# Performance work log

Measured on AMD Instinct MI355X. Metric: run time of the kernel, lower is better.

## Reference

```python
import jax, jax.numpy as jnp
import numpy as np

N = 1024
D_X = 128
D_Y = 128
NUM_STEPS = 200


def setup_inputs() -> dict:
    key = jax.random.key(0)
    k1, k2, k3, k4, k5 = jax.random.split(key, 5)
    init_samples_x = jax.random.normal(k1, (N, D_X), dtype=jnp.float32)
    init_samples_y = jax.random.normal(k2, (N, D_Y), dtype=jnp.float32)
    mean_final = jax.random.normal(k3, (D_X,), dtype=jnp.float32)
    # variance must be positive and bounded away from zero
    var_final = jax.random.uniform(k4, (D_X,), dtype=jnp.float32, minval=0.25, maxval=0.75)
    gammas = jnp.linspace(1e-3, 1e-2, NUM_STEPS, dtype=jnp.float32)
    # pre-generated per-step Gaussian noise (replaces torch.randn inside the loop)
    noise = jax.random.normal(k5, (NUM_STEPS, N, D_X), dtype=jnp.float32)
    return {
        "init_samples_x": init_samples_x,
        "init_samples_y": init_samples_y,
        "mean_final": mean_final,
        "var_final": var_final,
        "gammas": gammas,
        "noise": noise,
    }


def reference(init_samples_x, init_samples_y, mean_final, var_final, gammas, noise):
    """Faithful JAX port of Langevin.record_init_langevin.

    grad_gauss(x, m, v) = -(x - m) / v
    per step k:
        t_old = x + gamma_k * grad_gauss(x)
        x     = t_old + sqrt(2*gamma_k) * z_k
        t_new = x + gamma_k * grad_gauss(x)
        record x, y, t_old - t_new
    """
    num_steps = gammas.shape[0]
    n = init_samples_x.shape[0]

    def step(x, inp):
        gamma, z = inp
        t_old = x + gamma * (-(x - mean_final) / var_final)
        x_new = t_old + jnp.sqrt(2.0 * gamma) * z
        t_new = x_new + gamma * (-(x_new - mean_final) / var_final)
        return x_new, (x_new, t_old - t_new)

    _, (xs, outs) = jax.lax.scan(step, init_samples_x, (gammas, noise))
    # scan stacks along leading (step) axis -> [S, N, D]; match torch layout [N, S, D]
    x_tot = jnp.transpose(xs, (1, 0, 2))
    out = jnp.transpose(outs, (1, 0, 2))
    # y is constant across steps; the torch loop just replicates it
    y_tot = jnp.broadcast_to(init_samples_y[:, None, :], (n, num_steps, init_samples_y.shape[1]))
    steps_expanded = jnp.broadcast_to(
        jnp.arange(num_steps, dtype=jnp.int32)[None, :, None], (n, num_steps, 1)
    )
    return x_tot, y_tot, out, steps_expanded
```

## Files before the change

kernel.cpp:

```cpp
#include <hip/hip_runtime.h>
#include <math.h>

constexpr int N  = 1024;
constexpr int D  = 128;
constexpr int S  = 200;
constexpr int D2 = D / 2;

__global__ __launch_bounds__(256, 4) void langevin_kernel(
    const float2* __restrict__ x0,
    const float2* __restrict__ y0,
    const float2* __restrict__ mean,
    const float2* __restrict__ var,
    const float*  __restrict__ gammas,
    const float2* __restrict__ noise,
    float2* __restrict__ x_tot,
    float2* __restrict__ y_tot,
    float2* __restrict__ outp,
    float*  __restrict__ steps)
{
    __shared__ float sg[S];
    __shared__ float ss[S];
    for (int i = threadIdx.x; i < S; i += 256) {
        float g = gammas[i];
        sg[i] = g;
        ss[i] = sqrtf(2.0f * g);
    }
    __syncthreads();

    const int idx = blockIdx.x * 256 + threadIdx.x;
    const int n   = idx >> 6;
    const int dp  = idx & 63;

    float2 x       = x0[idx];
    const float2 y = y0[idx];
    const float2 m = mean[dp];
    const float2 v = var[dp];
    const float ivx = 1.0f / v.x;
    const float ivy = 1.0f / v.y;

    const float2* zp = noise + idx;
    float2* xq = x_tot + (size_t)n * (S * D2) + dp;
    float2* yq = y_tot + (size_t)n * (S * D2) + dp;
    float2* oq = outp  + (size_t)n * (S * D2) + dp;
    float*  sq = steps + (size_t)n * S;

    #pragma unroll 4
    for (int k = 0; k < S; ++k) {
        const float g = sg[k];
        const float s = ss[k];
        const float2 z = zp[(size_t)k * (N * D2)];

        const float gx = g * ivx;
        const float gy = g * ivy;

        const float tox = fmaf(-gx, x.x - m.x, x.x);
        const float toy = fmaf(-gy, x.y - m.y, x.y);
        x.x = fmaf(s, z.x, tox);
        x.y = fmaf(s, z.y, toy);
        const float tnx = fmaf(-gx, x.x - m.x, x.x);
        const float tny = fmaf(-gy, x.y - m.y, x.y);

        float2 o;
        o.x = tox - tnx;
        o.y = toy - tny;

        xq[(size_t)k * D2] = x;
        yq[(size_t)k * D2] = y;
        oq[(size_t)k * D2] = o;
        if (dp == 0) sq[k] = (float)k;
    }
}

extern "C" void kernel_launch(void* const* d_in, const int* in_sizes, int n_in,
                              void* d_out, int out_size, void* d_ws, size_t ws_size,
                              hipStream_t stream)
{
    const float* x0     = (const float*)d_in[0];
    const float* y0     = (const float*)d_in[1];
    const float* mean   = (const float*)d_in[2];
    const float* var    = (const float*)d_in[3];
    const float* gammas = (const float*)d_in[4];
    const float* noise  = (const float*)d_in[5];

    float* x_tot = (float*)d_out;
    float* y_tot = x_tot + (size_t)N * S * D;
    float* outp  = y_tot + (size_t)N * S * D;
    float* steps = outp  + (size_t)N * S * D;

    dim3 grid((N * D2) / 256);
    dim3 block(256);
    langevin_kernel<<<grid, block, 0, stream>>>(
        (const float2*)x0, (const float2*)y0, (const float2*)mean,
        (const float2*)var, gammas, (const float2*)noise,
        (float2*)x_tot, (float2*)y_tot, (float2*)outp, steps);
}
```

Before: 476.6 us.

## Split y/steps broadcast into separate blocks and software-prefetch noise with nontemporal ops

Adds N extra blocks that write the replicated y tensor with 16-byte nontemporal stores plus the step indices, removing that work from the Langevin chain threads. The chain threads now double-buffer noise loads eight steps ahead and use nontemporal loads and stores for the noise, x and out streams. The aim is better memory-level parallelism and less cache pollution on a purely bandwidth-bound kernel. Register use grows because of the prefetch buffers.

```diff
diff --git a/kernel.cpp b/kernel.cpp
--- a/kernel.cpp
+++ b/kernel.cpp
@@ -1,23 +1,45 @@
 #include <hip/hip_runtime.h>
 #include <math.h>
 
-constexpr int N  = 1024;
-constexpr int D  = 128;
-constexpr int S  = 200;
-constexpr int D2 = D / 2;
+constexpr int N   = 1024;
+constexpr int D   = 128;
+constexpr int S   = 200;
+constexpr int D2  = D / 2;
+constexpr int ND2 = N * D2;
+constexpr int CHAIN_BLOCKS = (N * D2) / 256;
+constexpr int PF  = 8;
+
+typedef float f2 __attribute__((ext_vector_type(2)));
+typedef float f4 __attribute__((ext_vector_type(4)));
 
 __global__ __launch_bounds__(256, 4) void langevin_kernel(
-    const float2* __restrict__ x0,
-    const float2* __restrict__ y0,
-    const float2* __restrict__ mean,
-    const float2* __restrict__ var,
-    const float*  __restrict__ gammas,
-    const float2* __restrict__ noise,
-    float2* __restrict__ x_tot,
-    float2* __restrict__ y_tot,
-    float2* __restrict__ outp,
-    float*  __restrict__ steps)
+    const f2* __restrict__ x0,
+    const f4* __restrict__ y0,
+    const f2* __restrict__ mean,
+    const f2* __restrict__ var,
+    const float* __restrict__ gammas,
+    const f2* __restrict__ noise,
+    f2* __restrict__ x_tot,
+    f4* __restrict__ y_tot,
+    f2* __restrict__ outp,
+    float* __restrict__ steps)
 {
+    if (blockIdx.x >= CHAIN_BLOCKS) {
+        const int n   = blockIdx.x - CHAIN_BLOCKS;
+        const int t   = threadIdx.x;
+        const int col = t & 31;
+        const int r0  = t >> 5;
+        const f4  yv  = y0[(size_t)n * 32 + col];
+        f4* yq = y_tot + (size_t)n * (S * 32);
+        #pragma unroll
+        for (int j = 0; j < S / 8; ++j) {
+            const int k = r0 + j * 8;
+            __builtin_nontemporal_store(yv, &yq[(size_t)k * 32 + col]);
+        }
+        if (t < S) steps[(size_t)n * S + t] = (float)t;
+        return;
+    }
+
     __shared__ float sg[S];
     __shared__ float ss[S];
     for (int i = threadIdx.x; i < S; i += 256) {
@@ -31,43 +53,53 @@
     const int n   = idx >> 6;
     const int dp  = idx & 63;
 
-    float2 x       = x0[idx];
-    const float2 y = y0[idx];
-    const float2 m = mean[dp];
-    const float2 v = var[dp];
+    f2 x        = x0[idx];
+    const f2 m  = mean[dp];
+    const f2 v  = var[dp];
     const float ivx = 1.0f / v.x;
     const float ivy = 1.0f / v.y;
 
-    const float2* zp = noise + idx;
-    float2* xq = x_tot + (size_t)n * (S * D2) + dp;
-    float2* yq = y_tot + (size_t)n * (S * D2) + dp;
-    float2* oq = outp  + (size_t)n * (S * D2) + dp;
-    float*  sq = steps + (size_t)n * S;
+    const f2* zp = noise + idx;
+    f2* xq = x_tot + (size_t)n * (S * D2) + dp;
+    f2* oq = outp  + (size_t)n * (S * D2) + dp;
 
-    #pragma unroll 4
-    for (int k = 0; k < S; ++k) {
-        const float g = sg[k];
-        const float s = ss[k];
-        const float2 z = zp[(size_t)k * (N * D2)];
+    f2 zb[PF];
+    #pragma unroll
+    for (int i = 0; i < PF; ++i)
+        zb[i] = __builtin_nontemporal_load(&zp[(size_t)i * ND2]);
 
-        const float gx = g * ivx;
-        const float gy = g * ivy;
+    #pragma unroll 1
+    for (int kb = 0; kb < S; kb += PF) {
+        f2 zn[PF];
+        if (kb + PF < S) {
+            #pragma unroll
+            for (int i = 0; i < PF; ++i)
+                zn[i] = __builtin_nontemporal_load(&zp[(size_t)(kb + PF + i) * ND2]);
+        }
+        #pragma unroll
+        for (int i = 0; i < PF; ++i) {
+            const int k = kb + i;
+            const float g = sg[k];
+            const float s = ss[k];
+            const float gx = g * ivx;
+            const float gy = g * ivy;
 
-        const float tox = fmaf(-gx, x.x - m.x, x.x);
-        const float toy = fmaf(-gy, x.y - m.y, x.y);
-        x.x = fmaf(s, z.x, tox);
-        x.y = fmaf(s, z.y, toy);
-        const float tnx = fmaf(-gx, x.x - m.x, x.x);
-        const float tny = fmaf(-gy, x.y - m.y, x.y);
+            const float tox = fmaf(-gx, x.x - m.x, x.x);
+            const float toy = fmaf(-gy, x.y - m.y, x.y);
+            x.x = fmaf(s, zb[i].x, tox);
+            x.y = fmaf(s, zb[i].y, toy);
+            const float tnx = fmaf(-gx, x.x - m.x, x.x);
+            const float tny = fmaf(-gy, x.y - m.y, x.y);
 
-        float2 o;
-        o.x = tox - tnx;
-        o.y = toy - tny;
+            f2 o;
+            o.x = tox - tnx;
+            o.y = toy - tny;
 
-        xq[(size_t)k * D2] = x;
-        yq[(size_t)k * D2] = y;
-        oq[(size_t)k * D2] = o;
-        if (dp == 0) sq[k] = (float)k;
+            __builtin_nontemporal_store(x, &xq[(size_t)k * D2]);
+            __builtin_nontemporal_store(o, &oq[(size_t)k * D2]);
+        }
+        #pragma unroll
+        for (int i = 0; i < PF; ++i) zb[i] = zn[i];
     }
 }
 
@@ -87,10 +119,10 @@
     float* outp  = y_tot + (size_t)N * S * D;
     float* steps = outp  + (size_t)N * S * D;
 
-    dim3 grid((N * D2) / 256);
+    dim3 grid(CHAIN_BLOCKS + N);
     dim3 block(256);
     langevin_kernel<<<grid, block, 0, stream>>>(
-        (const float2*)x0, (const float2*)y0, (const float2*)mean,
-        (const float2*)var, gammas, (const float2*)noise,
-        (float2*)x_tot, (float2*)y_tot, (float2*)outp, steps);
+        (const f2*)x0, (const f4*)y0, (const f2*)mean,
+        (const f2*)var, gammas, (const f2*)noise,
+        (f2*)x_tot, (f4*)y_tot, (f2*)outp, steps);
 }
```

Result: faster. 396.6 us, median of 2 (-16.8%).
